# Kernel optimization log

Measured on AMD Instinct MI355X. Metric: run time of the kernel, lower is better.

The kernel has to match this reference:

```python
import jax, jax.numpy as jnp
import numpy as np

B, N, E, F, FE = 4, 10000, 160000, 128, 16  # batch, nodes, edges, filters(=node feat dim), edge feat dim
EPS = 1e-3  # keras LayerNormalization default epsilon


def layernorm(x, gamma, beta):
    mu = jnp.mean(x, axis=-1, keepdims=True)
    var = jnp.mean(jnp.square(x - mu), axis=-1, keepdims=True)
    return (x - mu) * jax.lax.rsqrt(var + EPS) * gamma + beta


def setup_inputs() -> dict:
    key = jax.random.key(0)
    ks = jax.random.split(key, 8)
    nodes = jax.random.normal(ks[0], (B, N, F), dtype=jnp.float32)
    edge_features = jax.random.normal(ks[1], (B, E, FE), dtype=jnp.float32)
    edges = jax.random.randint(ks[2], (B, E, 2), 0, N, dtype=jnp.int32)
    edge_weights = jax.random.uniform(ks[3], (B, E, 1), dtype=jnp.float32)
    edge_dropout = jnp.ones((B, E, 2), dtype=jnp.float32)
    W_msg = jax.random.normal(ks[4], (2 * F + FE, F), dtype=jnp.float32) * 0.02
    b_msg = jnp.zeros((F,), jnp.float32)
    g_msg = jnp.ones((F,), jnp.float32)
    beta_msg = jnp.zeros((F,), jnp.float32)
    W_upd = jax.random.normal(ks[5], (2 * F, F), dtype=jnp.float32) * 0.02
    b_upd = jnp.zeros((F,), jnp.float32)
    g_upd = jnp.ones((F,), jnp.float32)
    beta_upd = jnp.zeros((F,), jnp.float32)
    return dict(nodes=nodes, edge_features=edge_features, edges=edges,
                edge_weights=edge_weights, edge_dropout=edge_dropout,
                W_msg=W_msg, b_msg=b_msg, g_msg=g_msg, beta_msg=beta_msg,
                W_upd=W_upd, b_upd=b_upd, g_upd=g_upd, beta_upd=beta_upd)


def reference(nodes, edge_features, edges, edge_weights, edge_dropout,
              W_msg, b_msg, g_msg, beta_msg, W_upd, b_upd, g_upd, beta_upd):
    n = nodes.shape[1]
    # gather both endpoints per edge: [B,E,2,F] -> [B,E,2F]
    gathered = jax.vmap(lambda nd, ed: nd[ed])(nodes, edges)
    msg_in = gathered.reshape(gathered.shape[0], gathered.shape[1], -1)
    msg_in = jnp.concatenate([msg_in, edge_features], axis=-1)
    # message MLP: Dense + GELU + LayerNorm
    h = jnp.einsum('bei,io->beo', msg_in, W_msg) + b_msg
    messages = layernorm(jax.nn.gelu(h, approximate=False), g_msg, beta_msg)
    weighted_messages = messages * edge_weights
    # scatter-sum to destination nodes (edge[:,1]), masked by dropout col 1
    dropped = weighted_messages * edge_dropout[..., 1:2]
    dst = edges[..., 1]
    aggregated = jax.vmap(lambda m, d: jax.ops.segment_sum(m, d, num_segments=n))(dropped, dst)
    # update: concat + Dense + GELU + LayerNorm
    combined = jnp.concatenate([nodes, aggregated], axis=-1)
    u = jnp.einsum('bni,io->bno', combined, W_upd) + b_upd
    updated_nodes = layernorm(jax.nn.gelu(u, approximate=False), g_upd, beta_upd)
    return updated_nodes
```

## Files before the change

kernel.cpp:

```cpp
#include <hip/hip_runtime.h>
#include <hip/hip_bf16.h>
#include <hip/hip_fp16.h>

#define BATCH   4
#define NNODES  10000
#define NEDGES  160000
#define FDIM    128
#define FEDIM   16
#define LNEPS   1e-3f
#define NTOTE   (BATCH * NEDGES)
#define NTOTN   (BATCH * NNODES)

typedef __attribute__((ext_vector_type(8))) short v8s;
typedef __attribute__((ext_vector_type(4))) float v4f;

#define AGG_BYTES   ((size_t)NTOTN * FDIM * 2)
#define CNT_OFF     AGG_BYTES
#define CNT_BYTES   ((size_t)NTOTN * 4)
#define CUR_OFF     (CNT_OFF + CNT_BYTES)
#define P_OFF       (CUR_OFF + CNT_BYTES)
#define P_BYTES     ((size_t)NTOTN * 256 * 2)
#define WTCAT_OFF   (P_OFF + P_BYTES)
#define WTUPD_OFF   (WTCAT_OFF + (size_t)256 * 128 * 2)
#define W3T_OFF     (WTUPD_OFF + (size_t)128 * 256 * 2)
#define REC_OFF     (W3T_OFF + (size_t)128 * 32 * 2)

static __device__ __forceinline__ unsigned short f2bf(float f) {
    __hip_bfloat16 h = __float2bfloat16(f);
    return *reinterpret_cast<unsigned short*>(&h);
}
static __device__ __forceinline__ float bfbits2f(unsigned bits16) {
    return __uint_as_float(bits16 << 16);
}

static __device__ __forceinline__ float gelu_f(float x) {
    float x2 = x * x;
    float z2 = 1.5957691216f * x * __builtin_fmaf(0.044715f, x2, 1.0f);
    float e  = __expf(z2);
    float r  = __builtin_amdgcn_rcpf(e + 1.0f);
    return __builtin_fmaf(-x, r, x);
}

static __device__ __forceinline__ bool is_bf16_mode(const void* gflag) {
    return ((*reinterpret_cast<const unsigned*>(gflag)) & 0xFFFFu) != 0u;
}
static __device__ __forceinline__ float ld_f(const void* p, long i, bool bf) {
    return bf ? (float)reinterpret_cast<const __hip_bfloat16*>(p)[i]
              : reinterpret_cast<const float*>(p)[i];
}
static __device__ __forceinline__ uint4 pack8(const float* p) {
    float4 f0 = *reinterpret_cast<const float4*>(p);
    float4 f1 = *reinterpret_cast<const float4*>(p + 4);
    uint4 o;
    o.x = f2bf(f0.x) | ((unsigned)f2bf(f0.y) << 16);
    o.y = f2bf(f0.z) | ((unsigned)f2bf(f0.w) << 16);
    o.z = f2bf(f1.x) | ((unsigned)f2bf(f1.y) << 16);
    o.w = f2bf(f1.z) | ((unsigned)f2bf(f1.w) << 16);
    return o;
}
static __device__ __forceinline__ uint4 h8_to_bf8(uint4 u) {
    unsigned w[4] = {u.x, u.y, u.z, u.w};
    uint4 o; unsigned r[4];
    #pragma unroll
    for (int q = 0; q < 4; q++) {
        __half lo = *reinterpret_cast<const __half*>(&w[q]);
        unsigned short hib = (unsigned short)(w[q] >> 16);
        __half hi = *reinterpret_cast<const __half*>(&hib);
        r[q] = f2bf(__half2float(lo)) | ((unsigned)f2bf(__half2float(hi)) << 16);
    }
    o.x = r[0]; o.y = r[1]; o.z = r[2]; o.w = r[3];
    return o;
}
static __device__ __forceinline__ uint4 shfl4(uint4 v, int src) {
    uint4 o;
    o.x = (unsigned)__shfl((int)v.x, src);
    o.y = (unsigned)__shfl((int)v.y, src);
    o.z = (unsigned)__shfl((int)v.z, src);
    o.w = (unsigned)__shfl((int)v.w, src);
    return o;
}

#define NCAT (256 * 128)
#define NUPD (128 * 256)
#define NW3  (128 * 32)
__global__ __launch_bounds__(256) void init_kernel(
    const void* __restrict__ Wmsg, const void* __restrict__ Wupd,
    const void* __restrict__ gflag,
    unsigned short* __restrict__ WtCat,
    unsigned short* __restrict__ WtUpd,
    unsigned short* __restrict__ W3t,
    uint4* __restrict__ aggz,
    uint4* __restrict__ cntz) {
    bool bf = is_bf16_mode(gflag);
    int i = blockIdx.x * 256 + threadIdx.x;
    aggz[i] = make_uint4(0, 0, 0, 0);
    if (i < (int)(CNT_BYTES / 16)) cntz[i] = make_uint4(0, 0, 0, 0);
    if (i < NCAT) {
        int n = i >> 7, k = i & 127;
        int src = (n < 128) ? (k * 128 + n) : ((128 + k) * 128 + (n - 128));
        WtCat[i] = bf ? reinterpret_cast<const unsigned short*>(Wmsg)[src]
                      : f2bf(reinterpret_cast<const float*>(Wmsg)[src]);
    } else if (i < NCAT + NUPD) {
        int j = i - NCAT;
        int n = j >> 8, c = j & 255;
        WtUpd[j] = bf ? reinterpret_cast<const unsigned short*>(Wupd)[c * 128 + n]
                      : f2bf(reinterpret_cast<const float*>(Wupd)[c * 128 + n]);
    } else if (i < NCAT + NUPD + NW3) {
        int j = i - NCAT - NUPD;
        int n = j >> 5, k = j & 31;
        W3t[j] = (k < 16) ? (bf ? reinterpret_cast<const unsigned short*>(Wmsg)[(256 + k) * 128 + n]
                                : f2bf(reinterpret_cast<const float*>(Wmsg)[(256 + k) * 128 + n]))
                          : (unsigned short)0;
    }
}

__global__ __launch_bounds__(1024) void scan_kernel(const int* __restrict__ counts,
                                                    int* __restrict__ cursor) {
    __shared__ int wsum[16];
    const int C = 40;
    int tid = threadIdx.x, lane = tid & 63, wave = tid >> 6;
    int lo = tid * C;
    const bool act = (lo < NTOTN);
    int vals[C];
    int s = 0;
    if (act) {
        #pragma unroll
        for (int q = 0; q < C / 4; q++) {
            int4 t4 = *reinterpret_cast<const int4*>(counts + lo + q * 4);
            vals[q * 4 + 0] = t4.x; vals[q * 4 + 1] = t4.y;
            vals[q * 4 + 2] = t4.z; vals[q * 4 + 3] = t4.w;
            s += t4.x + t4.y + t4.z + t4.w;
        }
    }
    int sc = s;
    #pragma unroll
    for (int off = 1; off < 64; off <<= 1) {
        int v = __shfl_up(sc, off);
        if (lane >= off) sc += v;
    }
    if (lane == 63) wsum[wave] = sc;
    __syncthreads();
    if (wave == 0 && lane < 16) {
        int t = wsum[lane];
        #pragma unroll
        for (int off = 1; off < 16; off <<= 1) {
            int v = __shfl_up(t, off);
            if (lane >= off) t += v;
        }
        wsum[lane] = t;
    }
    __syncthreads();
    int run = (wave > 0 ? wsum[wave - 1] : 0) + (sc - s);
    if (act) {
        #pragma unroll
        for (int q = 0; q < C / 4; q++) {
            int4 o;
            o.x = run; run += vals[q * 4 + 0];
            o.y = run; run += vals[q * 4 + 1];
            o.z = run; run += vals[q * 4 + 2];
            o.w = run; run += vals[q * 4 + 3];
            *reinterpret_cast<int4*>(cursor + lo + q * 4) = o;
        }
    }
}

__global__ __launch_bounds__(256) void sort_scatter(
    const int*  __restrict__ edges,
    const void* __restrict__ ew,
    const void* __restrict__ ed,
    const void* __restrict__ efeat,
    const void* __restrict__ gflag,
    int*        __restrict__ cursor,
    uint4*      __restrict__ rec4)
{
    const bool bf = is_bf16_mode(gflag);
    int gid = blockIdx.x * 256 + threadIdx.x;
    const int lane = threadIdx.x & 63, k = lane & 3, g4 = lane & ~3;
    int b = gid / NEDGES;
    long be = gid;
    int2 e = reinterpret_cast<const int2*>(edges)[gid];
    float w = ld_f(ew, be, bf) * ld_f(ed, be * 2 + 1, bf);
    uint4 R0, R1;
    if (bf) {
        const unsigned short* ep = reinterpret_cast<const unsigned short*>(efeat) + be * FEDIM;
        R0 = *reinterpret_cast<const uint4*>(ep);
        R1 = *reinterpret_cast<const uint4*>(ep + 8);
    } else {
        const float* ep = reinterpret_cast<const float*>(efeat) + be * FEDIM;
        R0 = pack8(ep);
        R1 = pack8(ep + 8);
    }
    uint4 R2 = make_uint4((unsigned)(b * NNODES + e.x),
                          (unsigned)(b * NNODES + e.y),
                          __float_as_uint(w),
                          (unsigned)gid);
    int pos = atomicAdd(&cursor[b * NNODES + e.y], 1);

    #pragma unroll
    for (int j = 0; j < 4; j++) {
        int src = g4 + j;
        uint4 a0 = shfl4(R0, src);
        uint4 a1 = shfl4(R1, src);
        uint4 a2 = shfl4(R2, src);
        int   pj = __shfl(pos, src);
        if (k < 3) {
            uint4 wv = (k == 0) ? a0 : (k == 1) ? a1 : a2;
            rec4[(size_t)pj * 4 + k] = wv;
        }
    }
}

__global__ __launch_bounds__(256) void pg_kernel(
    const void* __restrict__ nodes,
    const void* __restrict__ bmsg,
    const void* __restrict__ gflag,
    const unsigned short* __restrict__ Wt,
    const int*  __restrict__ edges,
    int*        __restrict__ counts,
    unsigned short*       __restrict__ P)
{
    const bool bf = is_bf16_mode(gflag);
    __shared__ unsigned short sW[128 * 40];
    __shared__ unsigned short sA[128 * 40];

    const int tid  = threadIdx.x;
    const int lane = tid & 63, wave = tid >> 6;
    const int c    = lane & 15, quad = lane >> 4;
    const int row0 = blockIdx.x * 128;
    const int half = blockIdx.y;
    const int NROWS = BATCH * NNODES;

    if (half == 0) {
        #pragma unroll
        for (int k = 0; k < 8; k++) {
            int g = blockIdx.x * 2048 + k * 256 + tid;
            if (g < NTOTE) {
                int2 e = reinterpret_cast<const int2*>(edges)[g];
                atomicAdd(&counts[(g / NEDGES) * NNODES + e.y], 1);
            }
        }
    }

    float bcol[8];
    #pragma unroll
    for (int nt = 0; nt < 8; nt++)
        bcol[nt] = (half == 0) ? ld_f(bmsg, nt * 16 + c, bf) : 0.f;

    v4f acc[2][8];
    #pragma unroll
    for (int mt = 0; mt < 2; mt++)
        #pragma unroll
        for (int nt = 0; nt < 8; nt++) { v4f z = {0.f, 0.f, 0.f, 0.f}; acc[mt][nt] = z; }

    for (int ks = 0; ks < 4; ks++) {
        #pragma unroll
        for (int q = tid; q < 512; q += 256) {
            int n = q >> 2, part = q & 3;
            *reinterpret_cast<uint4*>(&sW[n * 40 + part * 8]) =
                *reinterpret_cast<const uint4*>(Wt + (half * 128 + n) * 128 + ks * 32 + part * 8);
        }
        #pragma unroll
        for (int q = tid; q < 512; q += 256) {
            int t = q >> 2, part = q & 3;
            int row = row0 + t; if (row >= NROWS) row = NROWS - 1;
            long off = (size_t)row * FDIM + ks * 32 + part * 8;
            uint4 v = bf ? *reinterpret_cast<const uint4*>(reinterpret_cast<const unsigned short*>(nodes) + off)
                         : pack8(reinterpret_cast<const float*>(nodes) + off);
            *reinterpret_cast<uint4*>(&sA[t * 40 + part * 8]) = v;
        }
        __syncthreads();

        v8s a0 = *reinterpret_cast<const v8s*>(&sA[(wave * 32 + c) * 40 + quad * 8]);
        v8s a1 = *reinterpret_cast<const v8s*>(&sA[(wave * 32 + 16 + c) * 40 + quad * 8]);
        #pragma unroll
        for (int nt = 0; nt < 8; nt++) {
            v8s bfr = *reinterpret_cast<const v8s*>(&sW[(nt * 16 + c) * 40 + quad * 8]);
            acc[0][nt] = __builtin_amdgcn_mfma_f32_16x16x32_bf16(a0, bfr, acc[0][nt], 0, 0, 0);
            acc[1][nt] = __builtin_amdgcn_mfma_f32_16x16x32_bf16(a1, bfr, acc[1][nt], 0, 0, 0);
        }
        __syncthreads();
    }

    #pragma unroll
    for (int mt = 0; mt < 2; mt++)
        #pragma unroll
        for (int r = 0; r < 4; r++) {
            int row = row0 + wave * 32 + mt * 16 + quad * 4 + r;
            if (row < NROWS) {
                float v[8];
                #pragma unroll
                for (int nt = 0; nt < 8; nt++) v[nt] = acc[mt][nt][r] + bcol[nt];
                uint4 o;
                o.x = f2bf(v[0]) | ((unsigned)f2bf(v[1]) << 16);
                o.y = f2bf(v[2]) | ((unsigned)f2bf(v[3]) << 16);
                o.z = f2bf(v[4]) | ((unsigned)f2bf(v[5]) << 16);
                o.w = f2bf(v[6]) | ((unsigned)f2bf(v[7]) << 16);
                *reinterpret_cast<uint4*>(P + (size_t)row * 256 + half * 128 + c * 8) = o;
            }
        }
}

__global__ __launch_bounds__(256) void edge_kernel(
    const unsigned short* __restrict__ P,
    const uint4*          __restrict__ rec4,
    const unsigned short* __restrict__ W3t,
    const void* __restrict__ gmsg,
    const void* __restrict__ betamsg,
    __half*     __restrict__ agg)
{
    const bool bf = is_bf16_mode(gmsg);
    const int tid  = threadIdx.x;
    const int lane = tid & 63, wave = tid >> 6;
    const int c    = lane & 15, quad = lane >> 4;
    const int wbase = blockIdx.x * 512 + wave * 128;
    const int q0    = wbase + quad * 32;

    float gcol[8], becol[8];
    #pragma unroll
    for (int nt = 0; nt < 8; nt++) {
        gcol[nt]  = ld_f(gmsg, nt * 16 + c, bf);
        becol[nt] = ld_f(betamsg, nt * 16 + c, bf);
    }

    v8s bfrag[8];
    #pragma unroll
    for (int nt = 0; nt < 8; nt++)
        bfrag[nt] = *reinterpret_cast<const v8s*>(W3t + (nt * 16 + c) * 32 + quad * 8);

    const int prevd = (q0 == 0) ? -1 : (int)rec4[(size_t)(q0 - 1) * 4 + 2].y;
    const int nextd = (q0 + 32 >= NTOTE) ? -1 : (int)rec4[(size_t)(q0 + 32) * 4 + 2].y;

    const bool even = !(c & 1);
    float racc[8];
    int  cur = -1;
    bool owned = true;

    auto flushv = [&](int dstrow, bool plain) {
        __half* aout = agg + (size_t)dstrow * FDIM;
        #pragma unroll
        for (int np = 0; np < 4; np++) {
            int nt = np * 2;
            float t0 = __shfl_xor(racc[nt], 1);
            float t1 = __shfl_xor(racc[nt + 1], 1);
            __half2 v = even ? __floats2half2_rn(racc[nt], t0)
                             : __floats2half2_rn(t1, racc[nt + 1]);
            int hoff = even ? (nt * 16 + c) : ((nt + 1) * 16 + c - 1);
            if (plain) *reinterpret_cast<__half2*>(aout + hoff) = v;
            else       unsafeAtomicAdd(reinterpret_cast<__half2*>(aout + hoff), v);
        }
    };

    #pragma unroll 1
    for (int ph = 0; ph < 8; ph++) {
        v8s a = {0, 0, 0, 0, 0, 0, 0, 0};
        if (quad < 2) {
            int slot = wbase + (c >> 2) * 32 + ph * 4 + (c & 3);
            uint4 u = rec4[(size_t)slot * 4 + quad];
            a = *reinterpret_cast<v8s*>(&u);
        }
        v4f acc[8];
        #pragma unroll
        for (int nt = 0; nt < 8; nt++) { v4f z = {0.f, 0.f, 0.f, 0.f}; acc[nt] = z; }
        #pragma unroll
        for (int nt = 0; nt < 8; nt++)
            acc[nt] = __builtin_amdgcn_mfma_f32_16x16x32_bf16(a, bfrag[nt], acc[nt], 0, 0, 0);

        uint4 H[4];
        #pragma unroll
        for (int r = 0; r < 4; r++)
            H[r] = rec4[(size_t)(q0 + ph * 4 + r) * 4 + 2];
        uint4 U1[4], U2[4];
        #pragma unroll
        for (int r = 0; r < 4; r++) {
            U1[r] = *reinterpret_cast<const uint4*>(P + (size_t)H[r].x * 256 + c * 8);
            U2[r] = *reinterpret_cast<const uint4*>(P + (size_t)H[r].y * 256 + 128 + c * 8);
        }
        #pragma unroll
        for (int r = 0; r < 4; r++) {
            unsigned w1[4] = {U1[r].x, U1[r].y, U1[r].z, U1[r].w};
            unsigned w2[4] = {U2[r].x, U2[r].y, U2[r].z, U2[r].w};
            float h[8];
            #pragma unroll
            for (int q = 0; q < 4; q++) {
                h[q * 2]     = bfbits2f(w1[q] & 0xFFFFu) + bfbits2f(w2[q] & 0xFFFFu) + acc[q * 2][r];
                h[q * 2 + 1] = __uint_as_float(w1[q] & 0xFFFF0000u) + __uint_as_float(w2[q] & 0xFFFF0000u)
                               + acc[q * 2 + 1][r];
            }
            float s = 0.f, sq = 0.f;
            #pragma unroll
            for (int nt = 0; nt < 8; nt++) {
                float gg = gelu_f(h[nt]);
                h[nt] = gg; s += gg; sq += gg * gg;
            }
            #pragma unroll
            for (int off = 1; off < 16; off <<= 1) {
                s  += __shfl_xor(s, off);
                sq += __shfl_xor(sq, off);
            }
            float mu  = s * (1.0f / 128.0f);
            float var = sq * (1.0f / 128.0f) - mu * mu;
            float rs  = __builtin_amdgcn_rsqf(var + LNEPS);
            float wgt = __uint_as_float(H[r].z);
            int d = (int)H[r].y;
            if (d != cur) {
                if (cur >= 0) { flushv(cur, owned); owned = true; }
                else owned = (d != prevd);
                cur = d;
                #pragma unroll
                for (int nt = 0; nt < 8; nt++)
                    racc[nt] = ((h[nt] - mu) * rs * gcol[nt] + becol[nt]) * wgt;
            } else {
                #pragma unroll
                for (int nt = 0; nt < 8; nt++)
                    racc[nt] += ((h[nt] - mu) * rs * gcol[nt] + becol[nt]) * wgt;
            }
        }
    }
    flushv(cur, owned && (cur != nextd));
}

__global__ __launch_bounds__(256) void upd_kernel(
    const void* __restrict__ nodes,
    const __half* __restrict__ agg,
    const unsigned short* __restrict__ Wt,
    const void* __restrict__ bupd,
    const void* __restrict__ gupd,
    const void* __restrict__ beupd,
    void*       __restrict__ out)
{
    const bool bf = is_bf16_mode(gupd);
    __shared__ unsigned short sW[128 * 40];
    __shared__ unsigned short sA[64 * 40];

    const int tid  = threadIdx.x;
    const int lane = tid & 63, wave = tid >> 6;
    const int c    = lane & 15, quad = lane >> 4;
    const int row0 = blockIdx.x * 64;

    float bcol[8], gcol[8], becol[8];
    #pragma unroll
    for (int nt = 0; nt < 8; nt++) {
        int col = nt * 16 + c;
        bcol[nt]  = ld_f(bupd, col, bf);
        gcol[nt]  = ld_f(gupd, col, bf);
        becol[nt] = ld_f(beupd, col, bf);
    }

    v4f acc[8];
    #pragma unroll
    for (int nt = 0; nt < 8; nt++) { v4f z = {0.f, 0.f, 0.f, 0.f}; acc[nt] = z; }

    for (int ks = 0; ks < 8; ks++) {
        #pragma unroll
        for (int q = tid; q < 512; q += 256) {
            int n = q >> 2, part = q & 3;
            *reinterpret_cast<uint4*>(&sW[n * 40 + part * 8]) =
                *reinterpret_cast<const uint4*>(Wt + n * 256 + ks * 32 + part * 8);
        }
        {
            int t = tid >> 2, part = tid & 3;
            int row = row0 + t;
            uint4 v;
            if (ks < 4) {
                long off = (size_t)row * FDIM + ks * 32 + part * 8;
                v = bf ? *reinterpret_cast<const uint4*>(reinterpret_cast<const unsigned short*>(nodes) + off)
                       : pack8(reinterpret_cast<const float*>(nodes) + off);
            } else {
                uint4 u = *reinterpret_cast<const uint4*>(
                    reinterpret_cast<const unsigned short*>(agg) + (size_t)row * FDIM + (ks - 4) * 32 + part * 8);
                v = h8_to_bf8(u);
            }
            *reinterpret_cast<uint4*>(&sA[t * 40 + part * 8]) = v;
        }
        __syncthreads();

        v8s a0 = *reinterpret_cast<const v8s*>(&sA[(wave * 16 + c) * 40 + quad * 8]);
        #pragma unroll
        for (int nt = 0; nt < 8; nt++) {
            v8s bfr = *reinterpret_cast<const v8s*>(&sW[(nt * 16 + c) * 40 + quad * 8]);
            acc[nt] = __builtin_amdgcn_mfma_f32_16x16x32_bf16(a0, bfr, acc[nt], 0, 0, 0);
        }
        __syncthreads();
    }

    float s[4] = {0, 0, 0, 0}, sq[4] = {0, 0, 0, 0};
    #pragma unroll
    for (int nt = 0; nt < 8; nt++) {
        v4f v = acc[nt];
        #pragma unroll
        for (int r = 0; r < 4; r++) {
            float g = gelu_f(v[r] + bcol[nt]);
            v[r] = g;
            s[r] += g; sq[r] += g * g;
        }
        acc[nt] = v;
    }
    #pragma unroll
    for (int off = 1; off < 16; off <<= 1) {
        #pragma unroll
        for (int r = 0; r < 4; r++) {
            s[r]  += __shfl_xor(s[r], off);
            sq[r] += __shfl_xor(sq[r], off);
        }
    }
    #pragma unroll
    for (int r = 0; r < 4; r++) {
        float mu  = s[r] * (1.0f / 128.0f);
        float var = sq[r] * (1.0f / 128.0f) - mu * mu;
        float rs  = __builtin_amdgcn_rsqf(var + LNEPS);
        int row = row0 + wave * 16 + quad * 4 + r;
        #pragma unroll
        for (int nt = 0; nt < 8; nt++) {
            float y = (acc[nt][r] - mu) * rs * gcol[nt] + becol[nt];
            size_t oi = (size_t)row * FDIM + nt * 16 + c;
            if (bf) reinterpret_cast<__hip_bfloat16*>(out)[oi] = __float2bfloat16(y);
            else    reinterpret_cast<float*>(out)[oi] = y;
        }
    }
}

extern "C" void kernel_launch(void* const* d_in, const int* in_sizes, int n_in,
                              void* d_out, int out_size, void* d_ws, size_t ws_size,
                              hipStream_t stream)
{
    const void* nodes   = d_in[0];
    const void* efeat   = d_in[1];
    const int*  edges   = (const int*)d_in[2];
    const void* ew      = d_in[3];
    const void* ed      = d_in[4];
    const void* Wmsg    = d_in[5];
    const void* bmsg    = d_in[6];
    const void* gmsg    = d_in[7];
    const void* betamsg = d_in[8];
    const void* Wupd    = d_in[9];
    const void* bupd    = d_in[10];
    const void* gupd    = d_in[11];
    const void* betaupd = d_in[12];

    char* ws = (char*)d_ws;
    __half* agg          = (__half*)ws;
    int*    counts       = (int*)(ws + CNT_OFF);
    int*    cursor       = (int*)(ws + CUR_OFF);
    unsigned short* P    = (unsigned short*)(ws + P_OFF);
    unsigned short* WtCat= (unsigned short*)(ws + WTCAT_OFF);
    unsigned short* WtUpd= (unsigned short*)(ws + WTUPD_OFF);
    unsigned short* W3t  = (unsigned short*)(ws + W3T_OFF);
    uint4*          rec4 = (uint4*)(ws + REC_OFF);

    init_kernel<<<2500, 256, 0, stream>>>(
        Wmsg, Wupd, gmsg, WtCat, WtUpd, W3t, (uint4*)agg, (uint4*)counts);
    pg_kernel<<<dim3(313, 2), 256, 0, stream>>>(
        nodes, bmsg, gmsg, WtCat, edges, counts, P);
    scan_kernel<<<1, 1024, 0, stream>>>(counts, cursor);
    sort_scatter<<<NTOTE / 256, 256, 0, stream>>>(
        edges, ew, ed, efeat, gmsg, cursor, rec4);
    edge_kernel<<<NTOTE / 512, 256, 0, stream>>>(
        P, rec4, W3t, gmsg, betamsg, agg);
    upd_kernel<<<NTOTN / 64, 256, 0, stream>>>(
        nodes, agg, WtUpd, bupd, gupd, betaupd, d_out);
}
```

Baseline: 301.4 us.

## Fuse preprocessing, scan, projection GEMM and edge sort into one cooperative kernel

Replaces the init, pg, scan and sort_scatter launches with a single cooperative grid kernel. Its phases are separated by grid.sync: weight repack and zeroing, destination counting, a two-level block scan, and cursor write. After the scan, about 40% of blocks run the node-projection MFMA GEMM while the rest run the edge bucket scatter at the same time. The aim is to remove several launch gaps and the single-block scan, and to overlap the compute-bound GEMM with the memory- and atomic-bound scatter. The cost is five grid-wide barriers and grid-stride loops limited to a resident grid size, which may reduce parallelism in each phase.

Measured after the change: 478.5 us. +58.8%, slower.

```diff
diff --git a/kernel.cpp b/kernel.cpp
--- a/kernel.cpp
+++ b/kernel.cpp
@@ -1,6 +1,9 @@
 #include <hip/hip_runtime.h>
+#include <hip/hip_cooperative_groups.h>
 #include <hip/hip_bf16.h>
 #include <hip/hip_fp16.h>
+
+namespace cg = cooperative_groups;
 
 #define BATCH   4
 #define NNODES  10000
@@ -24,6 +27,7 @@
 #define WTUPD_OFF   (WTCAT_OFF + (size_t)256 * 128 * 2)
 #define W3T_OFF     (WTUPD_OFF + (size_t)128 * 256 * 2)
 #define REC_OFF     (W3T_OFF + (size_t)128 * 32 * 2)
+#define BSUM_OFF    (REC_OFF + (size_t)NTOTE * 64)
 
 static __device__ __forceinline__ unsigned short f2bf(float f) {
     __hip_bfloat16 h = __float2bfloat16(f);
@@ -83,221 +87,231 @@
 #define NCAT (256 * 128)
 #define NUPD (128 * 256)
 #define NW3  (128 * 32)
-__global__ __launch_bounds__(256) void init_kernel(
-    const void* __restrict__ Wmsg, const void* __restrict__ Wupd,
-    const void* __restrict__ gflag,
-    unsigned short* __restrict__ WtCat,
-    unsigned short* __restrict__ WtUpd,
-    unsigned short* __restrict__ W3t,
-    uint4* __restrict__ aggz,
-    uint4* __restrict__ cntz) {
-    bool bf = is_bf16_mode(gflag);
-    int i = blockIdx.x * 256 + threadIdx.x;
-    aggz[i] = make_uint4(0, 0, 0, 0);
-    if (i < (int)(CNT_BYTES / 16)) cntz[i] = make_uint4(0, 0, 0, 0);
-    if (i < NCAT) {
-        int n = i >> 7, k = i & 127;
-        int src = (n < 128) ? (k * 128 + n) : ((128 + k) * 128 + (n - 128));
-        WtCat[i] = bf ? reinterpret_cast<const unsigned short*>(Wmsg)[src]
-                      : f2bf(reinterpret_cast<const float*>(Wmsg)[src]);
-    } else if (i < NCAT + NUPD) {
-        int j = i - NCAT;
-        int n = j >> 8, c = j & 255;
-        WtUpd[j] = bf ? reinterpret_cast<const unsigned short*>(Wupd)[c * 128 + n]
-                      : f2bf(reinterpret_cast<const float*>(Wupd)[c * 128 + n]);
-    } else if (i < NCAT + NUPD + NW3) {
-        int j = i - NCAT - NUPD;
-        int n = j >> 5, k = j & 31;
-        W3t[j] = (k < 16) ? (bf ? reinterpret_cast<const unsigned short*>(Wmsg)[(256 + k) * 128 + n]
-                                : f2bf(reinterpret_cast<const float*>(Wmsg)[(256 + k) * 128 + n]))
-                          : (unsigned short)0;
-    }
-}
-
-__global__ __launch_bounds__(1024) void scan_kernel(const int* __restrict__ counts,
-                                                    int* __restrict__ cursor) {
-    __shared__ int wsum[16];
-    const int C = 40;
-    int tid = threadIdx.x, lane = tid & 63, wave = tid >> 6;
-    int lo = tid * C;
-    const bool act = (lo < NTOTN);
-    int vals[C];
-    int s = 0;
-    if (act) {
-        #pragma unroll
-        for (int q = 0; q < C / 4; q++) {
-            int4 t4 = *reinterpret_cast<const int4*>(counts + lo + q * 4);
-            vals[q * 4 + 0] = t4.x; vals[q * 4 + 1] = t4.y;
-            vals[q * 4 + 2] = t4.z; vals[q * 4 + 3] = t4.w;
-            s += t4.x + t4.y + t4.z + t4.w;
-        }
-    }
-    int sc = s;
-    #pragma unroll
-    for (int off = 1; off < 64; off <<= 1) {
-        int v = __shfl_up(sc, off);
-        if (lane >= off) sc += v;
-    }
-    if (lane == 63) wsum[wave] = sc;
-    __syncthreads();
-    if (wave == 0 && lane < 16) {
-        int t = wsum[lane];
-        #pragma unroll
-        for (int off = 1; off < 16; off <<= 1) {
-            int v = __shfl_up(t, off);
-            if (lane >= off) t += v;
-        }
-        wsum[lane] = t;
-    }
-    __syncthreads();
-    int run = (wave > 0 ? wsum[wave - 1] : 0) + (sc - s);
-    if (act) {
-        #pragma unroll
-        for (int q = 0; q < C / 4; q++) {
-            int4 o;
-            o.x = run; run += vals[q * 4 + 0];
-            o.y = run; run += vals[q * 4 + 1];
-            o.z = run; run += vals[q * 4 + 2];
-            o.w = run; run += vals[q * 4 + 3];
-            *reinterpret_cast<int4*>(cursor + lo + q * 4) = o;
-        }
-    }
-}
-
-__global__ __launch_bounds__(256) void sort_scatter(
+
+__global__ __launch_bounds__(256) void mega_kernel(
+    const void* __restrict__ nodes,
+    const void* __restrict__ efeat,
     const int*  __restrict__ edges,
     const void* __restrict__ ew,
     const void* __restrict__ ed,
-    const void* __restrict__ efeat,
-    const void* __restrict__ gflag,
-    int*        __restrict__ cursor,
-    uint4*      __restrict__ rec4)
-{
-    const bool bf = is_bf16_mode(gflag);
-    int gid = blockIdx.x * 256 + threadIdx.x;
-    const int lane = threadIdx.x & 63, k = lane & 3, g4 = lane & ~3;
-    int b = gid / NEDGES;
-    long be = gid;
-    int2 e = reinterpret_cast<const int2*>(edges)[gid];
-    float w = ld_f(ew, be, bf) * ld_f(ed, be * 2 + 1, bf);
-    uint4 R0, R1;
-    if (bf) {
-        const unsigned short* ep = reinterpret_cast<const unsigned short*>(efeat) + be * FEDIM;
-        R0 = *reinterpret_cast<const uint4*>(ep);
-        R1 = *reinterpret_cast<const uint4*>(ep + 8);
-    } else {
-        const float* ep = reinterpret_cast<const float*>(efeat) + be * FEDIM;
-        R0 = pack8(ep);
-        R1 = pack8(ep + 8);
-    }
-    uint4 R2 = make_uint4((unsigned)(b * NNODES + e.x),
-                          (unsigned)(b * NNODES + e.y),
-                          __float_as_uint(w),
-                          (unsigned)gid);
-    int pos = atomicAdd(&cursor[b * NNODES + e.y], 1);
-
-    #pragma unroll
-    for (int j = 0; j < 4; j++) {
-        int src = g4 + j;
-        uint4 a0 = shfl4(R0, src);
-        uint4 a1 = shfl4(R1, src);
-        uint4 a2 = shfl4(R2, src);
-        int   pj = __shfl(pos, src);
-        if (k < 3) {
-            uint4 wv = (k == 0) ? a0 : (k == 1) ? a1 : a2;
-            rec4[(size_t)pj * 4 + k] = wv;
-        }
-    }
-}
-
-__global__ __launch_bounds__(256) void pg_kernel(
-    const void* __restrict__ nodes,
+    const void* __restrict__ Wmsg,
     const void* __restrict__ bmsg,
     const void* __restrict__ gflag,
-    const unsigned short* __restrict__ Wt,
-    const int*  __restrict__ edges,
-    int*        __restrict__ counts,
-    unsigned short*       __restrict__ P)
+    const void* __restrict__ Wupd,
+    char*       __restrict__ ws)
 {
+    cg::grid_group grid = cg::this_grid();
     const bool bf = is_bf16_mode(gflag);
+    const int  tid = threadIdx.x;
+    const int  G = gridDim.x;
+    const long gstride = (long)G * 256;
+    const long gtid = (long)blockIdx.x * 256 + tid;
+
+    __half* agg           = (__half*)ws;
+    int* counts           = (int*)(ws + CNT_OFF);
+    int* cursor           = (int*)(ws + CUR_OFF);
+    unsigned short* P     = (unsigned short*)(ws + P_OFF);
+    unsigned short* WtCat = (unsigned short*)(ws + WTCAT_OFF);
+    unsigned short* WtUpd = (unsigned short*)(ws + WTUPD_OFF);
+    unsigned short* W3t   = (unsigned short*)(ws + W3T_OFF);
+    uint4* rec4           = (uint4*)(ws + REC_OFF);
+    int* bsum             = (int*)(ws + BSUM_OFF);
+
     __shared__ unsigned short sW[128 * 40];
     __shared__ unsigned short sA[128 * 40];
-
-    const int tid  = threadIdx.x;
-    const int lane = tid & 63, wave = tid >> 6;
-    const int c    = lane & 15, quad = lane >> 4;
-    const int row0 = blockIdx.x * 128;
-    const int half = blockIdx.y;
-    const int NROWS = BATCH * NNODES;
-
-    if (half == 0) {
-        #pragma unroll
-        for (int k = 0; k < 8; k++) {
-            int g = blockIdx.x * 2048 + k * 256 + tid;
-            if (g < NTOTE) {
-                int2 e = reinterpret_cast<const int2*>(edges)[g];
-                atomicAdd(&counts[(g / NEDGES) * NNODES + e.y], 1);
-            }
-        }
-    }
-
-    float bcol[8];
-    #pragma unroll
-    for (int nt = 0; nt < 8; nt++)
-        bcol[nt] = (half == 0) ? ld_f(bmsg, nt * 16 + c, bf) : 0.f;
-
-    v4f acc[2][8];
-    #pragma unroll
-    for (int mt = 0; mt < 2; mt++)
-        #pragma unroll
-        for (int nt = 0; nt < 8; nt++) { v4f z = {0.f, 0.f, 0.f, 0.f}; acc[mt][nt] = z; }
-
-    for (int ks = 0; ks < 4; ks++) {
-        #pragma unroll
-        for (int q = tid; q < 512; q += 256) {
-            int n = q >> 2, part = q & 3;
-            *reinterpret_cast<uint4*>(&sW[n * 40 + part * 8]) =
-                *reinterpret_cast<const uint4*>(Wt + (half * 128 + n) * 128 + ks * 32 + part * 8);
-        }
-        #pragma unroll
-        for (int q = tid; q < 512; q += 256) {
-            int t = q >> 2, part = q & 3;
-            int row = row0 + t; if (row >= NROWS) row = NROWS - 1;
-            long off = (size_t)row * FDIM + ks * 32 + part * 8;
-            uint4 v = bf ? *reinterpret_cast<const uint4*>(reinterpret_cast<const unsigned short*>(nodes) + off)
-                         : pack8(reinterpret_cast<const float*>(nodes) + off);
-            *reinterpret_cast<uint4*>(&sA[t * 40 + part * 8]) = v;
-        }
+    __shared__ int wsh[4];
+
+    {
+        const uint4 z4 = make_uint4(0, 0, 0, 0);
+        uint4* aggz = (uint4*)agg;
+        uint4* cntz = (uint4*)counts;
+        for (long i = gtid; i < (long)(AGG_BYTES / 16); i += gstride) {
+            aggz[i] = z4;
+            if (i < (long)(CNT_BYTES / 16)) cntz[i] = z4;
+            if (i < NCAT) {
+                int n = (int)i >> 7, k = (int)i & 127;
+                int src = (n < 128) ? (k * 128 + n) : ((128 + k) * 128 + (n - 128));
+                WtCat[i] = bf ? reinterpret_cast<const unsigned short*>(Wmsg)[src]
+                              : f2bf(reinterpret_cast<const float*>(Wmsg)[src]);
+            } else if (i < NCAT + NUPD) {
+                int j = (int)i - NCAT;
+                int n = j >> 8, c = j & 255;
+                WtUpd[j] = bf ? reinterpret_cast<const unsigned short*>(Wupd)[c * 128 + n]
+                              : f2bf(reinterpret_cast<const float*>(Wupd)[c * 128 + n]);
+            } else if (i < NCAT + NUPD + NW3) {
+                int j = (int)i - NCAT - NUPD;
+                int n = j >> 5, k = j & 31;
+                W3t[j] = (k < 16) ? (bf ? reinterpret_cast<const unsigned short*>(Wmsg)[(256 + k) * 128 + n]
+                                        : f2bf(reinterpret_cast<const float*>(Wmsg)[(256 + k) * 128 + n]))
+                                  : (unsigned short)0;
+            }
+        }
+    }
+    grid.sync();
+
+    for (long g = gtid; g < NTOTE; g += gstride) {
+        int2 e = reinterpret_cast<const int2*>(edges)[g];
+        atomicAdd(&counts[(int)(g / NEDGES) * NNODES + e.y], 1);
+    }
+    grid.sync();
+
+    int myval = 0, myinc = 0;
+    {
+        myval = (gtid < NTOTN) ? counts[gtid] : 0;
+        int lane = tid & 63, wv = tid >> 6;
+        int sc = myval;
+        #pragma unroll
+        for (int off = 1; off < 64; off <<= 1) {
+            int t = __shfl_up(sc, off);
+            if (lane >= off) sc += t;
+        }
+        if (lane == 63) wsh[wv] = sc;
         __syncthreads();
-
-        v8s a0 = *reinterpret_cast<const v8s*>(&sA[(wave * 32 + c) * 40 + quad * 8]);
-        v8s a1 = *reinterpret_cast<const v8s*>(&sA[(wave * 32 + 16 + c) * 40 + quad * 8]);
-        #pragma unroll
-        for (int nt = 0; nt < 8; nt++) {
-            v8s bfr = *reinterpret_cast<const v8s*>(&sW[(nt * 16 + c) * 40 + quad * 8]);
-            acc[0][nt] = __builtin_amdgcn_mfma_f32_16x16x32_bf16(a0, bfr, acc[0][nt], 0, 0, 0);
-            acc[1][nt] = __builtin_amdgcn_mfma_f32_16x16x32_bf16(a1, bfr, acc[1][nt], 0, 0, 0);
-        }
+        int add = 0;
+        #pragma unroll
+        for (int j = 0; j < 3; j++) add += (j < wv) ? wsh[j] : 0;
+        myinc = sc + add;
+        if (tid == 255) bsum[blockIdx.x] = myinc;
         __syncthreads();
     }
-
-    #pragma unroll
-    for (int mt = 0; mt < 2; mt++)
-        #pragma unroll
-        for (int r = 0; r < 4; r++) {
-            int row = row0 + wave * 32 + mt * 16 + quad * 4 + r;
-            if (row < NROWS) {
-                float v[8];
-                #pragma unroll
-                for (int nt = 0; nt < 8; nt++) v[nt] = acc[mt][nt][r] + bcol[nt];
-                uint4 o;
-                o.x = f2bf(v[0]) | ((unsigned)f2bf(v[1]) << 16);
-                o.y = f2bf(v[2]) | ((unsigned)f2bf(v[3]) << 16);
-                o.z = f2bf(v[4]) | ((unsigned)f2bf(v[5]) << 16);
-                o.w = f2bf(v[6]) | ((unsigned)f2bf(v[7]) << 16);
-                *reinterpret_cast<uint4*>(P + (size_t)row * 256 + half * 128 + c * 8) = o;
-            }
-        }
+    grid.sync();
+
+    if (blockIdx.x == 0) {
+        int ch = (G + 255) >> 8;
+        int lo = tid * ch, hi = lo + ch;
+        if (lo > G) lo = G;
+        if (hi > G) hi = G;
+        int s = 0;
+        for (int i = lo; i < hi; i++) s += bsum[i];
+        int lane = tid & 63, wv = tid >> 6;
+        int sc = s;
+        #pragma unroll
+        for (int off = 1; off < 64; off <<= 1) {
+            int t = __shfl_up(sc, off);
+            if (lane >= off) sc += t;
+        }
+        if (lane == 63) wsh[wv] = sc;
+        __syncthreads();
+        int add = 0;
+        #pragma unroll
+        for (int j = 0; j < 3; j++) add += (j < wv) ? wsh[j] : 0;
+        int run = sc + add - s;
+        for (int i = lo; i < hi; i++) { int v = bsum[i]; bsum[i] = run; run += v; }
+    }
+    grid.sync();
+
+    if (gtid < NTOTN) cursor[gtid] = bsum[blockIdx.x] + myinc - myval;
+    grid.sync();
+
+    const int PGB = (G * 2) / 5;
+    if (blockIdx.x < PGB) {
+        const int lane = tid & 63, wave = tid >> 6;
+        const int c = lane & 15, quad = lane >> 4;
+        for (int lb = blockIdx.x; lb < 626; lb += PGB) {
+            const int bx = lb >> 1, half = lb & 1;
+            const int row0 = bx * 128;
+            float bcol[8];
+            #pragma unroll
+            for (int nt = 0; nt < 8; nt++)
+                bcol[nt] = (half == 0) ? ld_f(bmsg, nt * 16 + c, bf) : 0.f;
+
+            v4f acc[2][8];
+            #pragma unroll
+            for (int mt = 0; mt < 2; mt++)
+                #pragma unroll
+                for (int nt = 0; nt < 8; nt++) { v4f z = {0.f, 0.f, 0.f, 0.f}; acc[mt][nt] = z; }
+
+            for (int ks = 0; ks < 4; ks++) {
+                #pragma unroll
+                for (int q = tid; q < 512; q += 256) {
+                    int n = q >> 2, part = q & 3;
+                    *reinterpret_cast<uint4*>(&sW[n * 40 + part * 8]) =
+                        *reinterpret_cast<const uint4*>(WtCat + (half * 128 + n) * 128 + ks * 32 + part * 8);
+                }
+                #pragma unroll
+                for (int q = tid; q < 512; q += 256) {
+                    int t = q >> 2, part = q & 3;
+                    int row = row0 + t; if (row >= NTOTN) row = NTOTN - 1;
+                    long off = (size_t)row * FDIM + ks * 32 + part * 8;
+                    uint4 v = bf ? *reinterpret_cast<const uint4*>(reinterpret_cast<const unsigned short*>(nodes) + off)
+                                 : pack8(reinterpret_cast<const float*>(nodes) + off);
+                    *reinterpret_cast<uint4*>(&sA[t * 40 + part * 8]) = v;
+                }
+                __syncthreads();
+
+                v8s a0 = *reinterpret_cast<const v8s*>(&sA[(wave * 32 + c) * 40 + quad * 8]);
+                v8s a1 = *reinterpret_cast<const v8s*>(&sA[(wave * 32 + 16 + c) * 40 + quad * 8]);
+                #pragma unroll
+                for (int nt = 0; nt < 8; nt++) {
+                    v8s bfr = *reinterpret_cast<const v8s*>(&sW[(nt * 16 + c) * 40 + quad * 8]);
+                    acc[0][nt] = __builtin_amdgcn_mfma_f32_16x16x32_bf16(a0, bfr, acc[0][nt], 0, 0, 0);
+                    acc[1][nt] = __builtin_amdgcn_mfma_f32_16x16x32_bf16(a1, bfr, acc[1][nt], 0, 0, 0);
+                }
+                __syncthreads();
+            }
+
+            #pragma unroll
+            for (int mt = 0; mt < 2; mt++)
+                #pragma unroll
+                for (int r = 0; r < 4; r++) {
+                    int row = row0 + wave * 32 + mt * 16 + quad * 4 + r;
+                    if (row < NTOTN) {
+                        float v[8];
+                        #pragma unroll
+                        for (int nt = 0; nt < 8; nt++) v[nt] = acc[mt][nt][r] + bcol[nt];
+                        uint4 o;
+                        o.x = f2bf(v[0]) | ((unsigned)f2bf(v[1]) << 16);
+                        o.y = f2bf(v[2]) | ((unsigned)f2bf(v[3]) << 16);
+                        o.z = f2bf(v[4]) | ((unsigned)f2bf(v[5]) << 16);
+                        o.w = f2bf(v[6]) | ((unsigned)f2bf(v[7]) << 16);
+                        *reinterpret_cast<uint4*>(P + (size_t)row * 256 + half * 128 + c * 8) = o;
+                    }
+                }
+        }
+    } else {
+        const int lane = tid & 63, k = lane & 3, g4 = lane & ~3;
+        const long sbase = (long)(blockIdx.x - PGB) * 256 + tid;
+        const long sstride = (long)(G - PGB) * 256;
+        const int  niter = (int)((NTOTE + sstride - 1) / sstride);
+        for (int it = 0; it < niter; it++) {
+            long g = sbase + (long)it * sstride;
+            bool act = g < NTOTE;
+            long gc = act ? g : (NTOTE - 1);
+            int b = (int)(gc / NEDGES);
+            int2 e = reinterpret_cast<const int2*>(edges)[gc];
+            float w = ld_f(ew, gc, bf) * ld_f(ed, gc * 2 + 1, bf);
+            uint4 R0, R1;
+            if (bf) {
+                const unsigned short* ep = reinterpret_cast<const unsigned short*>(efeat) + gc * FEDIM;
+                R0 = *reinterpret_cast<const uint4*>(ep);
+                R1 = *reinterpret_cast<const uint4*>(ep + 8);
+            } else {
+                const float* ep = reinterpret_cast<const float*>(efeat) + gc * FEDIM;
+                R0 = pack8(ep);
+                R1 = pack8(ep + 8);
+            }
+            uint4 R2 = make_uint4((unsigned)(b * NNODES + e.x),
+                                  (unsigned)(b * NNODES + e.y),
+                                  __float_as_uint(w),
+                                  (unsigned)gc);
+            int pos = 0;
+            if (act) pos = atomicAdd(&cursor[b * NNODES + e.y], 1);
+
+            #pragma unroll
+            for (int j = 0; j < 4; j++) {
+                int src = g4 + j;
+                uint4 a0 = shfl4(R0, src);
+                uint4 a1 = shfl4(R1, src);
+                uint4 a2 = shfl4(R2, src);
+                int   pj = __shfl(pos, src);
+                long  gsrc = g + (j - k);
+                if (k < 3 && gsrc < NTOTE) {
+                    uint4 wv = (k == 0) ? a0 : (k == 1) ? a1 : a2;
+                    rec4[(size_t)pj * 4 + k] = wv;
+                }
+            }
+        }
+    }
 }
 
 __global__ __launch_bounds__(256) void edge_kernel(
@@ -539,23 +553,36 @@
 
     char* ws = (char*)d_ws;
     __half* agg          = (__half*)ws;
-    int*    counts       = (int*)(ws + CNT_OFF);
-    int*    cursor       = (int*)(ws + CUR_OFF);
     unsigned short* P    = (unsigned short*)(ws + P_OFF);
-    unsigned short* WtCat= (unsigned short*)(ws + WTCAT_OFF);
     unsigned short* WtUpd= (unsigned short*)(ws + WTUPD_OFF);
     unsigned short* W3t  = (unsigned short*)(ws + W3T_OFF);
     uint4*          rec4 = (uint4*)(ws + REC_OFF);
 
-    init_kernel<<<2500, 256, 0, stream>>>(
-        Wmsg, Wupd, gmsg, WtCat, WtUpd, W3t, (uint4*)agg, (uint4*)counts);
-    pg_kernel<<<dim3(313, 2), 256, 0, stream>>>(
-        nodes, bmsg, gmsg, WtCat, edges, counts, P);
-    scan_kernel<<<1, 1024, 0, stream>>>(counts, cursor);
-    sort_scatter<<<NTOTE / 256, 256, 0, stream>>>(
-        edges, ew, ed, efeat, gmsg, cursor, rec4);
+    static int coopG = 0;
+    if (coopG == 0) {
+        int nb = 0;
+        if (hipOccupancyMaxActiveBlocksPerMultiprocessor(&nb, mega_kernel, 256, 0) != hipSuccess || nb < 1)
+            nb = 1;
+        int ncu = 0;
+        if (hipDeviceGetAttribute(&ncu, hipDeviceAttributeMultiprocessorCount, 0) != hipSuccess || ncu <= 0)
+            ncu = 256;
+        long g = (long)nb * ncu;
+        if (g > 4096) g = 4096;
+        if (g < 160)  g = 160;
+        coopG = (int)g;
+    }
+
+    const void* m_nodes = nodes; const void* m_efeat = efeat; const int* m_edges = edges;
+    const void* m_ew = ew; const void* m_ed = ed; const void* m_Wmsg = Wmsg;
+    const void* m_bmsg = bmsg; const void* m_g = gmsg; const void* m_Wupd = Wupd;
+    char* m_ws = ws;
+    void* margs[10] = {(void*)&m_nodes, (void*)&m_efeat, (void*)&m_edges, (void*)&m_ew,
+                       (void*)&m_ed, (void*)&m_Wmsg, (void*)&m_bmsg, (void*)&m_g,
+                       (void*)&m_Wupd, (void*)&m_ws};
+
+    hipLaunchCooperativeKernel(mega_kernel, dim3(coopG), dim3(256), margs, 0, stream);
     edge_kernel<<<NTOTE / 512, 256, 0, stream>>>(
         P, rec4, W3t, gmsg, betamsg, agg);
     upd_kernel<<<NTOTN / 64, 256, 0, stream>>>(
-        nodes, agg, WtUpd, bupd, gupd, betaupd, d_out);
-}
+        nodes, agg, (unsigned short*)WtUpd, bupd, gupd, betaupd, d_out);
+}
```
